# Kernel optimization log

Hardware: AMD Instinct MI355X
Metric: run time of the kernel (lower is better)

Reference implementation:

```python
import jax, jax.numpy as jnp
import numpy as np

B, L, D, H = 2, 4096, 512, 8
DK = D // H
SCALE = 1.0 / float(np.sqrt(DK))


def setup_inputs() -> dict:
    key = jax.random.key(0)
    k1, k2, k3 = jax.random.split(key, 3)
    x = jax.random.normal(k1, (B, L, D), dtype=jnp.float32)
    w_qkv = jax.random.normal(k2, (3 * D, D), dtype=jnp.float32) * 0.02
    w_o = jax.random.normal(k3, (D, D), dtype=jnp.float32) * 0.02
    return {"x": x, "w_qkv": w_qkv, "w_o": w_o}


def reference(x, w_qkv, w_o):
    b, l, d = x.shape
    # qkv projection: Linear(d, 3d, bias=False) -> x @ W^T
    qkv = (x @ w_qkv.T).reshape(b, l, 3, H, DK).transpose(2, 0, 3, 1, 4)  # [3,B,H,L,dk]
    q, k, v = qkv[0], qkv[1], qkv[2]
    # naive O(L^2) attention (faithful to source)
    scores = jnp.einsum("bhld,bhmd->bhlm", q, k) * SCALE  # [B,H,L,L]
    attn = jax.nn.softmax(scores, axis=-1)
    ctx = jnp.einsum("bhlm,bhmd->bhld", attn, v)  # [B,H,L,dk]
    ctx = ctx.transpose(0, 2, 1, 3).reshape(b, l, d)
    return ctx @ w_o.T
```

## Files before the change

kernel.cpp:

```cpp
#include <hip/hip_runtime.h>


#define Bq 2
#define Lq 4096
#define Dq 512
#define Hq 8
#define DKq 64

using short8  = __attribute__((ext_vector_type(8))) short;
using short4v = __attribute__((ext_vector_type(4))) short;
using ushort8 = __attribute__((ext_vector_type(8))) unsigned short;
using float4v = __attribute__((ext_vector_type(4))) float;
using half4   = __attribute__((ext_vector_type(4))) _Float16;
typedef unsigned short u16;
typedef unsigned int   u32;

__device__ __forceinline__ u16 f2bf(float f) {
    u32 u = __float_as_uint(f);
    u += 0x7fffu + ((u >> 16) & 1u);
    return (u16)(u >> 16);
}

__device__ __forceinline__ float4v mfma16(short8 a, short8 b, float4v c) {
    return __builtin_amdgcn_mfma_f32_16x16x32_bf16(a, b, c, 0, 0, 0);
}

__device__ __forceinline__ float4v mfma1k(short4v a, short4v b, float4v c) {
#if __has_builtin(__builtin_amdgcn_mfma_f32_16x16x16bf16_1k)
    return __builtin_amdgcn_mfma_f32_16x16x16bf16_1k(a, b, c, 0, 0, 0);
#else
    float4v d;
    asm volatile("v_mfma_f32_16x16x16_bf16 %0, %1, %2, %3"
                 : "=v"(d) : "v"(a), "v"(b), "v"(c));
    return d;
#endif
}

__device__ __forceinline__ void gload_lds16(const u16* g, u16* l) {
    __builtin_amdgcn_global_load_lds(
        (const __attribute__((address_space(1))) unsigned int*)g,
        (__attribute__((address_space(3))) unsigned int*)l,
        16, 0, 0);
}

__global__ __launch_bounds__(256) void castall(const float* __restrict__ x,
                                               const float* __restrict__ wq,
                                               const float* __restrict__ wo,
                                               u16* __restrict__ xb,
                                               u16* __restrict__ wqb,
                                               u16* __restrict__ wob) {
    int g = blockIdx.x;
    const float* s; u16* d; int base;
    if (g < 4096)      { s = x;  d = xb;  base = g * 1024; }
    else if (g < 4864) { s = wq; d = wqb; base = (g - 4096) * 1024; }
    else               { s = wo; d = wob; base = (g - 4864) * 1024; }
    int i = base + threadIdx.x * 4;
    float4 f = *(const float4*)&s[i];
    ushort4 o;
    o.x = f2bf(f.x); o.y = f2bf(f.y); o.z = f2bf(f.z); o.w = f2bf(f.w);
    *(ushort4*)&d[i] = o;
}

__global__ __launch_bounds__(256) void qkv_gemm(const u16* __restrict__ A,
                                                const u16* __restrict__ Bw,
                                                u16* __restrict__ qb,
                                                u16* __restrict__ kb,
                                                u16* __restrict__ vt) {
    __shared__ __align__(16) union {
        struct { u16 A[128 * 64]; u16 B[128 * 64]; } s;
        u16 epi[128 * 134];
    } sm;
    const int m0 = blockIdx.x * 128, n0 = blockIdx.y * 128;
    const int tid = threadIdx.x, w = tid >> 6, lane = tid & 63;
    const int l15 = lane & 15, quad = lane >> 4;
    const int wy = w & 1, wx = w >> 1;
    const int r8 = lane >> 3, c8 = lane & 7, csw = c8 ^ r8;
    const int sw = l15 & 7;

    float4v acc[4][4];
    float4v zero = {0.f, 0.f, 0.f, 0.f};
#pragma unroll
    for (int mi = 0; mi < 4; mi++)
#pragma unroll
        for (int ni = 0; ni < 4; ni++) acc[mi][ni] = zero;

    for (int k0 = 0; k0 < 512; k0 += 64) {
#pragma unroll
        for (int i = 0; i < 4; i++) {
            int row = w * 32 + i * 8;
            gload_lds16(&A[(size_t)(m0 + row + r8) * 512 + k0 + csw * 8], &sm.s.A[row * 64]);
            gload_lds16(&Bw[(size_t)(n0 + row + r8) * 512 + k0 + csw * 8], &sm.s.B[row * 64]);
        }
        __syncthreads();
        short8 af0[4], af1[4], bf0[4], bf1[4];
#pragma unroll
        for (int t = 0; t < 4; t++) {
            int rowA = wy * 64 + t * 16 + l15;
            af0[t] = *(const short8*)&sm.s.A[rowA * 64 + ((quad ^ sw) * 8)];
            af1[t] = *(const short8*)&sm.s.A[rowA * 64 + (((quad + 4) ^ sw) * 8)];
            int rowB = wx * 64 + t * 16 + l15;
            bf0[t] = *(const short8*)&sm.s.B[rowB * 64 + ((quad ^ sw) * 8)];
            bf1[t] = *(const short8*)&sm.s.B[rowB * 64 + (((quad + 4) ^ sw) * 8)];
        }
#pragma unroll
        for (int mi = 0; mi < 4; mi++)
#pragma unroll
            for (int ni = 0; ni < 4; ni++) {
                acc[mi][ni] = mfma16(af0[mi], bf0[ni], acc[mi][ni]);
                acc[mi][ni] = mfma16(af1[mi], bf1[ni], acc[mi][ni]);
            }
        __syncthreads();
    }

    const int sel = n0 >> 9;
    if (sel < 2) {
        const float sc = (sel == 0) ? 0.125f : 1.0f;
#pragma unroll
        for (int mi = 0; mi < 4; mi++)
#pragma unroll
            for (int ni = 0; ni < 4; ni++)
#pragma unroll
                for (int r = 0; r < 4; r++)
                    sm.epi[(wy * 64 + mi * 16 + quad * 4 + r) * 134 + wx * 64 + ni * 16 + l15] =
                        f2bf(acc[mi][ni][r] * sc);
        __syncthreads();
        u16* tgt = (sel == 0) ? qb : kb;
#pragma unroll
        for (int i = 0; i < 8; i++) {
            int flat = i * 2048 + tid * 8;
            int row = flat >> 7, col = flat & 127;
            ushort8 vv = *(const ushort8*)&sm.epi[row * 134 + col];
            int dg = (n0 & 511) + col, h = dg >> 6, dk = dg & 63;
            int mm = m0 + row, b = mm >> 12, l = mm & 4095;
            *(ushort8*)&tgt[((size_t)(b * Hq + h) * Lq + l) * DKq + dk] = vv;
        }
    } else {
#pragma unroll
        for (int mi = 0; mi < 4; mi++)
#pragma unroll
            for (int ni = 0; ni < 4; ni++) {
                ushort4 v4;
                v4.x = f2bf(acc[mi][ni][0]); v4.y = f2bf(acc[mi][ni][1]);
                v4.z = f2bf(acc[mi][ni][2]); v4.w = f2bf(acc[mi][ni][3]);
                *(ushort4*)&sm.epi[(wx * 64 + ni * 16 + l15) * 134 + wy * 64 + mi * 16 + quad * 4] = v4;
            }
        __syncthreads();
#pragma unroll
        for (int i = 0; i < 8; i++) {
            int flat = i * 2048 + tid * 8;
            int vrow = flat >> 7, vcol = flat & 127;
            ushort8 vv = *(const ushort8*)&sm.epi[vrow * 134 + vcol];
            int dg = (n0 & 511) + vrow, h = dg >> 6, dk = dg & 63;
            int mm = m0 + vcol, b = mm >> 12, l = mm & 4095;
            *(ushort8*)&vt[((size_t)(b * Hq + h) * DKq + dk) * Lq + l] = vv;
        }
    }
}

__global__ __launch_bounds__(256) void attn_kern(const u16* __restrict__ qb,
                                                 const u16* __restrict__ kb,
                                                 const u16* __restrict__ vt,
                                                 _Float16* __restrict__ op0,
                                                 _Float16* __restrict__ op1,
                                                 float* __restrict__ denp) {
    __shared__ __align__(16) u16 KV[2][2][64 * 64];
    const int g = blockIdx.x;
    const int bh = (g & 7) * 2 + ((g >> 3) & 1);
    const int rest = g >> 4;
    const int split = rest & 1;
    const int q0 = (rest >> 1) * 128;
    const int tid = threadIdx.x;
    const int w = tid >> 6, lane = tid & 63, l15 = lane & 15, quad = lane >> 4;
    const int wq = w & 1, wk = w >> 1;
    const int r8 = lane >> 3, c8 = lane & 7, csw = c8 ^ r8;
    const int sw = l15 & 7;

    const u16* qbase = qb + (size_t)bh * Lq * DKq;
    const u16* kbase = kb + (size_t)bh * Lq * DKq;
    const u16* vbase = vt + (size_t)bh * DKq * Lq;

    short8 aq0[4], aq1[4];
#pragma unroll
    for (int s = 0; s < 4; s++) {
        int qrow = q0 + wq * 64 + s * 16 + l15;
        aq0[s] = *(const short8*)&qbase[(size_t)qrow * DKq + quad * 8];
        aq1[s] = *(const short8*)&qbase[(size_t)qrow * DKq + 32 + quad * 8];
    }

    short4v ones4 = {(short)0x3F80, (short)0x3F80, (short)0x3F80, (short)0x3F80};
    float4v zero = {0.f, 0.f, 0.f, 0.f};
    float4v oacc[4][4], den[4];
#pragma unroll
    for (int s = 0; s < 4; s++) {
        den[s] = zero;
#pragma unroll
        for (int n = 0; n < 4; n++) oacc[s][n] = zero;
    }

    const int j0base = split * 2048;
    {
        int j0 = j0base;
        if (w < 2) {
#pragma unroll
            for (int i = 0; i < 4; i++) {
                int base = w * 32 + i * 8;
                gload_lds16(&kbase[(size_t)(j0 + base + r8) * DKq + csw * 8], &KV[0][0][base * 64]);
            }
        } else {
#pragma unroll
            for (int i = 0; i < 4; i++) {
                int base = (w - 2) * 32 + i * 8;
                gload_lds16(&vbase[(size_t)(base + r8) * Lq + j0 + csw * 8], &KV[0][1][base * 64]);
            }
        }
    }

    int p = 0;
    for (int jt = 0; jt < 32; jt++) {
        __syncthreads();
        if (jt < 31) {
            int j0 = j0base + (jt + 1) * 64;
            if (w < 2) {
#pragma unroll
                for (int i = 0; i < 4; i++) {
                    int base = w * 32 + i * 8;
                    gload_lds16(&kbase[(size_t)(j0 + base + r8) * DKq + csw * 8], &KV[p ^ 1][0][base * 64]);
                }
            } else {
#pragma unroll
                for (int i = 0; i < 4; i++) {
                    int base = (w - 2) * 32 + i * 8;
                    gload_lds16(&vbase[(size_t)(base + r8) * Lq + j0 + csw * 8], &KV[p ^ 1][1][base * 64]);
                }
            }
        }
        const u16* Kb = KV[p][0];
        const u16* Vb = KV[p][1];
#pragma unroll
        for (int nkk = 0; nkk < 2; nkk++) {
            int krow = wk * 32 + nkk * 16 + l15;
            short8 k0 = *(const short8*)&Kb[krow * 64 + ((quad ^ sw) * 8)];
            short8 k1 = *(const short8*)&Kb[krow * 64 + (((quad + 4) ^ sw) * 8)];
            int kc = ((wk * 4 + nkk * 2 + (quad >> 1)) ^ sw) * 8 + (quad & 1) * 4;
            short4v vf[4];
#pragma unroll
            for (int n = 0; n < 4; n++)
                vf[n] = *(const short4v*)&Vb[(n * 16 + l15) * 64 + kc];
#pragma unroll
            for (int s = 0; s < 4; s++) {
                float4v sv = mfma16(k0, aq0[s], zero);
                sv = mfma16(k1, aq1[s], sv);
                u32 u0 = __float_as_uint(__expf(sv[0])) + 0x8000u;
                u32 u1 = __float_as_uint(__expf(sv[1])) + 0x8000u;
                u32 u2 = __float_as_uint(__expf(sv[2])) + 0x8000u;
                u32 u3 = __float_as_uint(__expf(sv[3])) + 0x8000u;
                union { uint2 u; short4v s4; } cv;
                cv.u.x = __builtin_amdgcn_perm(u1, u0, 0x07060302u);
                cv.u.y = __builtin_amdgcn_perm(u3, u2, 0x07060302u);
                short4v pf = cv.s4;
                den[s] = mfma1k(pf, ones4, den[s]);
#pragma unroll
                for (int n = 0; n < 4; n++)
                    oacc[s][n] = mfma1k(pf, vf[n], oacc[s][n]);
            }
        }
        p ^= 1;
    }
    __syncthreads();

    float4v* sc4 = (float4v*)&KV[0][0][0];
    if (wk == 1) {
        float4v* dst = sc4 + (size_t)(wq * 64 + lane) * 13;
#pragma unroll
        for (int s = 0; s < 4; s++) dst[s] = den[s];
#pragma unroll
        for (int s = 0; s < 2; s++)
#pragma unroll
            for (int n = 0; n < 4; n++) dst[4 + s * 4 + n] = oacc[s][n];
    }
    __syncthreads();
    if (wk == 0) {
        float4v* src = sc4 + (size_t)(wq * 64 + lane) * 13;
#pragma unroll
        for (int s = 0; s < 4; s++) den[s] += src[s];
#pragma unroll
        for (int s = 0; s < 2; s++)
#pragma unroll
            for (int n = 0; n < 4; n++) oacc[s][n] += src[4 + s * 4 + n];
    }
    __syncthreads();
    if (wk == 1) {
        float4v* dst = sc4 + (size_t)(wq * 64 + lane) * 9;
#pragma unroll
        for (int s = 2; s < 4; s++)
#pragma unroll
            for (int n = 0; n < 4; n++) dst[(s - 2) * 4 + n] = oacc[s][n];
    }
    __syncthreads();
    if (wk == 0) {
        float4v* src = sc4 + (size_t)(wq * 64 + lane) * 9;
#pragma unroll
        for (int s = 2; s < 4; s++)
#pragma unroll
            for (int n = 0; n < 4; n++) oacc[s][n] += src[(s - 2) * 4 + n];

        _Float16* op = split ? op1 : op0;
#pragma unroll
        for (int s = 0; s < 4; s++)
#pragma unroll
            for (int r = 0; r < 4; r++) {
                float dv = den[s][r];
                float rd = __builtin_amdgcn_rcpf(dv);
                int row = q0 + wq * 64 + s * 16 + quad * 4 + r;
                if (l15 == 0) denp[(size_t)(split * 16 + bh) * Lq + row] = dv;
#pragma unroll
                for (int n = 0; n < 4; n++)
                    op[((size_t)bh * Lq + row) * DKq + n * 16 + l15] =
                        (_Float16)(oacc[s][n][r] * rd);
            }
    }
}

__global__ __launch_bounds__(256) void combine(const _Float16* __restrict__ op0,
                                               const _Float16* __restrict__ op1,
                                               const float* __restrict__ denp,
                                               u16* __restrict__ ctxq) {
    int t = blockIdx.x * 256 + threadIdx.x;
    int dk4 = t & 15, l = (t >> 4) & 4095, bh = t >> 16;
    size_t r0 = (size_t)bh * Lq + l;
    half4 h0 = *(const half4*)&op0[r0 * DKq + dk4 * 4];
    half4 h1 = *(const half4*)&op1[r0 * DKq + dk4 * 4];
    float d0 = denp[r0];
    float d1 = denp[(size_t)(16 + bh) * Lq + l];
    float rs = __builtin_amdgcn_rcpf(d0 + d1);
    int b = bh >> 3, h = bh & 7;
    ushort4 o;
    o.x = f2bf(((float)h0.x * d0 + (float)h1.x * d1) * rs);
    o.y = f2bf(((float)h0.y * d0 + (float)h1.y * d1) * rs);
    o.z = f2bf(((float)h0.z * d0 + (float)h1.z * d1) * rs);
    o.w = f2bf(((float)h0.w * d0 + (float)h1.w * d1) * rs);
    *(ushort4*)&ctxq[((size_t)(b * Lq + l)) * Dq + h * DKq + dk4 * 4] = o;
}

__global__ __launch_bounds__(256) void out_gemm(const u16* __restrict__ A,
                                                const u16* __restrict__ Bw,
                                                float* __restrict__ out) {
    __shared__ __align__(16) union {
        struct { u16 A[128 * 64]; u16 B[128 * 64]; } s;
        float fepi[64 * 132];
    } sm;
    const int m0 = blockIdx.x * 128, n0 = blockIdx.y * 128;
    const int tid = threadIdx.x, w = tid >> 6, lane = tid & 63;
    const int l15 = lane & 15, quad = lane >> 4;
    const int wy = w & 1, wx = w >> 1;
    const int r8 = lane >> 3, c8 = lane & 7, csw = c8 ^ r8;
    const int sw = l15 & 7;

    float4v acc[4][4];
    float4v zero = {0.f, 0.f, 0.f, 0.f};
#pragma unroll
    for (int mi = 0; mi < 4; mi++)
#pragma unroll
        for (int ni = 0; ni < 4; ni++) acc[mi][ni] = zero;

    for (int k0 = 0; k0 < 512; k0 += 64) {
#pragma unroll
        for (int i = 0; i < 4; i++) {
            int row = w * 32 + i * 8;
            gload_lds16(&A[(size_t)(m0 + row + r8) * 512 + k0 + csw * 8], &sm.s.A[row * 64]);
            gload_lds16(&Bw[(size_t)(n0 + row + r8) * 512 + k0 + csw * 8], &sm.s.B[row * 64]);
        }
        __syncthreads();
        short8 af0[4], af1[4], bf0[4], bf1[4];
#pragma unroll
        for (int t = 0; t < 4; t++) {
            int rowA = wy * 64 + t * 16 + l15;
            af0[t] = *(const short8*)&sm.s.A[rowA * 64 + ((quad ^ sw) * 8)];
            af1[t] = *(const short8*)&sm.s.A[rowA * 64 + (((quad + 4) ^ sw) * 8)];
            int rowB = wx * 64 + t * 16 + l15;
            bf0[t] = *(const short8*)&sm.s.B[rowB * 64 + ((quad ^ sw) * 8)];
            bf1[t] = *(const short8*)&sm.s.B[rowB * 64 + (((quad + 4) ^ sw) * 8)];
        }
#pragma unroll
        for (int mi = 0; mi < 4; mi++)
#pragma unroll
            for (int ni = 0; ni < 4; ni++) {
                acc[mi][ni] = mfma16(af0[mi], bf0[ni], acc[mi][ni]);
                acc[mi][ni] = mfma16(af1[mi], bf1[ni], acc[mi][ni]);
            }
        __syncthreads();
    }

#pragma unroll
    for (int ph = 0; ph < 2; ph++) {
#pragma unroll
        for (int mh = 0; mh < 2; mh++) {
            int mi = ph * 2 + mh;
            int lr = wy * 32 + mh * 16 + quad * 4;
#pragma unroll
            for (int ni = 0; ni < 4; ni++)
#pragma unroll
                for (int r = 0; r < 4; r++)
                    sm.fepi[(lr + r) * 132 + wx * 64 + ni * 16 + l15] = acc[mi][ni][r];
        }
        __syncthreads();
#pragma unroll
        for (int i = 0; i < 8; i++) {
            int flat = i * 1024 + tid * 4;
            int lrow = flat >> 7, col = flat & 127;
            float4 vv = *(const float4*)&sm.fepi[lrow * 132 + col];
            int m = (lrow & 31) + (lrow >> 5) * 64 + ph * 32;
            *(float4*)&out[(size_t)(m0 + m) * 512 + n0 + col] = vv;
        }
        __syncthreads();
    }
}

extern "C" void kernel_launch(void* const* d_in, const int* in_sizes, int n_in,
                              void* d_out, int out_size, void* d_ws, size_t ws_size,
                              hipStream_t stream) {
    const float* x     = (const float*)d_in[0];
    const float* w_qkv = (const float*)d_in[1];
    const float* w_o   = (const float*)d_in[2];
    float* out = (float*)d_out;

    const size_t N_X   = (size_t)Bq * Lq * Dq;
    const size_t N_WQ  = (size_t)3 * Dq * Dq;
    const size_t N_WO  = (size_t)Dq * Dq;
    const size_t N_QKV = (size_t)Bq * Hq * Lq * DKq;

    u16* xb  = (u16*)d_ws;
    u16* wqb = xb + N_X;
    u16* wob = wqb + N_WQ;
    u16* qb  = wob + N_WO;
    u16* kb  = qb + N_QKV;
    u16* vt  = kb + N_QKV;
    u16* o1r = vt + N_QKV;

    _Float16* op0  = (_Float16*)xb;
    _Float16* op1  = (_Float16*)o1r;
    float*    denp = (float*)wqb;
    u16*      ctxq = qb;

    castall<<<dim3(5120), 256, 0, stream>>>(x, w_qkv, w_o, xb, wqb, wob);
    qkv_gemm<<<dim3(64, 12), 256, 0, stream>>>(xb, wqb, qb, kb, vt);
    attn_kern<<<dim3(1024), 256, 0, stream>>>(qb, kb, vt, op0, op1, denp);
    combine<<<dim3(4096), 256, 0, stream>>>(op0, op1, denp, ctxq);
    out_gemm<<<dim3(64, 4), 256, 0, stream>>>(ctxq, wob, out);
}
```

Measured before the change: 207.3 us.

## Stage softmax P through LDS to use 16x16x32 MFMA for PV

The attention kernel now writes exp'd bf16 probabilities to a per-wave LDS tile, then reads them back as 8-wide fragments. This lets the PV product and the denominator use the larger 16x16x32 bf16 MFMA instead of 16x16x16 ones, halving the number of MFMA issues for that stage. It adds LDS writes and reads per tile plus extra LDS footprint, and sets a min-occupancy launch bound of 3 blocks. The reduction scratch strides shrink from 13/9 to 12/8, which may add bank conflicts.

```diff
diff --git a/kernel.cpp b/kernel.cpp
--- a/kernel.cpp
+++ b/kernel.cpp
@@ -6,9 +6,9 @@
 #define Dq 512
 #define Hq 8
 #define DKq 64
+#define PST 40
 
 using short8  = __attribute__((ext_vector_type(8))) short;
-using short4v = __attribute__((ext_vector_type(4))) short;
 using ushort8 = __attribute__((ext_vector_type(8))) unsigned short;
 using float4v = __attribute__((ext_vector_type(4))) float;
 using half4   = __attribute__((ext_vector_type(4))) _Float16;
@@ -23,17 +23,6 @@
 
 __device__ __forceinline__ float4v mfma16(short8 a, short8 b, float4v c) {
     return __builtin_amdgcn_mfma_f32_16x16x32_bf16(a, b, c, 0, 0, 0);
-}
-
-__device__ __forceinline__ float4v mfma1k(short4v a, short4v b, float4v c) {
-#if __has_builtin(__builtin_amdgcn_mfma_f32_16x16x16bf16_1k)
-    return __builtin_amdgcn_mfma_f32_16x16x16bf16_1k(a, b, c, 0, 0, 0);
-#else
-    float4v d;
-    asm volatile("v_mfma_f32_16x16x16_bf16 %0, %1, %2, %3"
-                 : "=v"(d) : "v"(a), "v"(b), "v"(c));
-    return d;
-#endif
 }
 
 __device__ __forceinline__ void gload_lds16(const u16* g, u16* l) {
@@ -157,13 +146,14 @@
     }
 }
 
-__global__ __launch_bounds__(256) void attn_kern(const u16* __restrict__ qb,
-                                                 const u16* __restrict__ kb,
-                                                 const u16* __restrict__ vt,
-                                                 _Float16* __restrict__ op0,
-                                                 _Float16* __restrict__ op1,
-                                                 float* __restrict__ denp) {
+__global__ __launch_bounds__(256, 3) void attn_kern(const u16* __restrict__ qb,
+                                                    const u16* __restrict__ kb,
+                                                    const u16* __restrict__ vt,
+                                                    _Float16* __restrict__ op0,
+                                                    _Float16* __restrict__ op1,
+                                                    float* __restrict__ denp) {
     __shared__ __align__(16) u16 KV[2][2][64 * 64];
+    __shared__ __align__(16) u16 Ps[4][64 * PST];
     const int g = blockIdx.x;
     const int bh = (g & 7) * 2 + ((g >> 3) & 1);
     const int rest = g >> 4;
@@ -187,7 +177,10 @@
         aq1[s] = *(const short8*)&qbase[(size_t)qrow * DKq + 32 + quad * 8];
     }
 
-    short4v ones4 = {(short)0x3F80, (short)0x3F80, (short)0x3F80, (short)0x3F80};
+    short8 ones8;
+#pragma unroll
+    for (int j = 0; j < 8; j++) ones8[j] = (short)0x3F80;
+
     float4v zero = {0.f, 0.f, 0.f, 0.f};
     float4v oacc[4][4], den[4];
 #pragma unroll
@@ -197,7 +190,9 @@
         for (int n = 0; n < 4; n++) oacc[s][n] = zero;
     }
 
+    u16* Pw = &Ps[w][0];
     const int j0base = split * 2048;
+
     {
         int j0 = j0base;
         if (w < 2) {
@@ -236,16 +231,12 @@
         }
         const u16* Kb = KV[p][0];
         const u16* Vb = KV[p][1];
-#pragma unroll
-        for (int nkk = 0; nkk < 2; nkk++) {
-            int krow = wk * 32 + nkk * 16 + l15;
+
+#pragma unroll
+        for (int kg = 0; kg < 2; kg++) {
+            int krow = wk * 32 + kg * 16 + l15;
             short8 k0 = *(const short8*)&Kb[krow * 64 + ((quad ^ sw) * 8)];
             short8 k1 = *(const short8*)&Kb[krow * 64 + (((quad + 4) ^ sw) * 8)];
-            int kc = ((wk * 4 + nkk * 2 + (quad >> 1)) ^ sw) * 8 + (quad & 1) * 4;
-            short4v vf[4];
-#pragma unroll
-            for (int n = 0; n < 4; n++)
-                vf[n] = *(const short4v*)&Vb[(n * 16 + l15) * 64 + kc];
 #pragma unroll
             for (int s = 0; s < 4; s++) {
                 float4v sv = mfma16(k0, aq0[s], zero);
@@ -254,15 +245,24 @@
                 u32 u1 = __float_as_uint(__expf(sv[1])) + 0x8000u;
                 u32 u2 = __float_as_uint(__expf(sv[2])) + 0x8000u;
                 u32 u3 = __float_as_uint(__expf(sv[3])) + 0x8000u;
-                union { uint2 u; short4v s4; } cv;
-                cv.u.x = __builtin_amdgcn_perm(u1, u0, 0x07060302u);
-                cv.u.y = __builtin_amdgcn_perm(u3, u2, 0x07060302u);
-                short4v pf = cv.s4;
-                den[s] = mfma1k(pf, ones4, den[s]);
-#pragma unroll
-                for (int n = 0; n < 4; n++)
-                    oacc[s][n] = mfma1k(pf, vf[n], oacc[s][n]);
-            }
+                uint2 pv;
+                pv.x = __builtin_amdgcn_perm(u1, u0, 0x07060302u);
+                pv.y = __builtin_amdgcn_perm(u3, u2, 0x07060302u);
+                *(uint2*)&Pw[(s * 16 + l15) * PST + kg * 16 + quad * 4] = pv;
+            }
+        }
+
+        short8 vf[4];
+#pragma unroll
+        for (int n = 0; n < 4; n++)
+            vf[n] = *(const short8*)&Vb[(n * 16 + l15) * 64 + (((wk * 4 + quad) ^ sw) * 8)];
+#pragma unroll
+        for (int s = 0; s < 4; s++) {
+            short8 ap = *(const short8*)&Pw[(s * 16 + l15) * PST + quad * 8];
+            den[s] = mfma16(ap, ones8, den[s]);
+#pragma unroll
+            for (int n = 0; n < 4; n++)
+                oacc[s][n] = mfma16(ap, vf[n], oacc[s][n]);
         }
         p ^= 1;
     }
@@ -270,7 +270,7 @@
 
     float4v* sc4 = (float4v*)&KV[0][0][0];
     if (wk == 1) {
-        float4v* dst = sc4 + (size_t)(wq * 64 + lane) * 13;
+        float4v* dst = sc4 + (size_t)(wq * 64 + lane) * 12;
 #pragma unroll
         for (int s = 0; s < 4; s++) dst[s] = den[s];
 #pragma unroll
@@ -280,7 +280,7 @@
     }
     __syncthreads();
     if (wk == 0) {
-        float4v* src = sc4 + (size_t)(wq * 64 + lane) * 13;
+        float4v* src = sc4 + (size_t)(wq * 64 + lane) * 12;
 #pragma unroll
         for (int s = 0; s < 4; s++) den[s] += src[s];
 #pragma unroll
@@ -290,7 +290,7 @@
     }
     __syncthreads();
     if (wk == 1) {
-        float4v* dst = sc4 + (size_t)(wq * 64 + lane) * 9;
+        float4v* dst = sc4 + (size_t)(wq * 64 + lane) * 8;
 #pragma unroll
         for (int s = 2; s < 4; s++)
 #pragma unroll
@@ -298,7 +298,7 @@
     }
     __syncthreads();
     if (wk == 0) {
-        float4v* src = sc4 + (size_t)(wq * 64 + lane) * 9;
+        float4v* src = sc4 + (size_t)(wq * 64 + lane) * 8;
 #pragma unroll
         for (int s = 2; s < 4; s++)
 #pragma unroll
```

Result: slower. 221.4 us (+6.8%).
